# Kernel tuning notes

Hardware: AMD Instinct MI355X
Metric: run time of the kernel (lower is better)

## Reference

```python
import jax, jax.numpy as jnp
import numpy as np

N = 10000      # nodes
E = 160000     # edges (before self loops)
F_IN = 512     # in_features
F_OUT = 256    # out_features
SLOPE = 0.2    # LeakyReLU negative slope (PyG GATConv default)
EPS = 1e-12    # F.normalize eps


def setup_inputs() -> dict:
    key = jax.random.key(0)
    ks = jax.random.split(key, 14)
    feat = jax.random.normal(ks[0], (N, F_IN), jnp.float32)
    feat_a = jax.random.normal(ks[1], (N, F_IN), jnp.float32)
    edge_index = jax.random.randint(ks[2], (2, E), 0, N, dtype=jnp.int32)
    # binary neighborhood mask; diagonal set so every row has >=1 entry
    gn = (jax.random.uniform(ks[3], (N, N)) < 0.0016).astype(jnp.float32)
    graph_neigh = gn.at[jnp.arange(N), jnp.arange(N)].set(1.0)
    s1 = 1.0 / np.sqrt(F_IN)
    s2 = 1.0 / np.sqrt(F_OUT)
    return {
        "feat": feat,
        "feat_a": feat_a,
        "edge_index": edge_index,
        "graph_neigh": graph_neigh,
        # conv1: GATConv(F_IN -> F_OUT, heads=1)
        "W1": jax.random.normal(ks[4], (F_OUT, F_IN), jnp.float32) * s1,
        "att_src1": jax.random.normal(ks[5], (F_OUT,), jnp.float32) * s2,
        "att_dst1": jax.random.normal(ks[6], (F_OUT,), jnp.float32) * s2,
        "b1": jnp.zeros((F_OUT,), jnp.float32),
        # conv2: GATConv(F_OUT -> F_IN, heads=1)
        "W2": jax.random.normal(ks[7], (F_IN, F_OUT), jnp.float32) * s2,
        "att_src2": jax.random.normal(ks[8], (F_IN,), jnp.float32) * s1,
        "att_dst2": jax.random.normal(ks[9], (F_IN,), jnp.float32) * s1,
        "b2": jnp.zeros((F_IN,), jnp.float32),
        # discriminator bilinear
        "Wd": jax.random.normal(ks[10], (F_OUT, F_OUT), jnp.float32) * s2,
        "bd": jnp.zeros((), jnp.float32),
    }


def _gat_conv(x, src, dst, W, a_src, a_dst, b):
    # PyG GATConv, heads=1, concat=True, add_self_loops already applied.
    h = x @ W.T                       # [N, out]
    a_s = h @ a_src                   # [N]
    a_d = h @ a_dst                   # [N]
    e = a_s[src] + a_d[dst]           # [E+N]
    e = jnp.where(e > 0, e, SLOPE * e)  # leaky relu
    m = jax.ops.segment_max(e, dst, num_segments=N)
    p = jnp.exp(e - m[dst])
    s = jax.ops.segment_sum(p, dst, num_segments=N)
    coef = p / s[dst]                 # per-dst softmax over incoming edges
    out = jax.ops.segment_sum(coef[:, None] * h[src], dst, num_segments=N)
    return out + b


def reference(feat, feat_a, edge_index, graph_neigh, W1, att_src1, att_dst1, b1,
              W2, att_src2, att_dst2, b2, Wd, bd):
    loops = jnp.arange(N, dtype=edge_index.dtype)
    src = jnp.concatenate([edge_index[0], loops])
    dst = jnp.concatenate([edge_index[1], loops])

    z = _gat_conv(feat, src, dst, W1, att_src1, att_dst1, b1)      # [N, F_OUT]
    hiden_emb = z
    h = _gat_conv(z, src, dst, W2, att_src2, att_dst2, b2)         # [N, F_IN]
    emb = jax.nn.relu(z)
    z_a = _gat_conv(feat_a, src, dst, W1, att_src1, att_dst1, b1)
    emb_a = jax.nn.relu(z_a)

    def readout(e):
        vsum = graph_neigh @ e                                     # [N, F_OUT]
        row_sum = graph_neigh.sum(axis=1, keepdims=True)
        g = vsum / row_sum
        g = g / jnp.maximum(jnp.linalg.norm(g, axis=1, keepdims=True), EPS)
        return jax.nn.sigmoid(g)

    g = readout(emb)
    g_a = readout(emb_a)

    def bilin(x1, x2):
        return jnp.einsum('nd,de,ne->n', x1, Wd, x2)[:, None] + bd

    ret = jnp.concatenate([bilin(emb, g), bilin(emb_a, g)], axis=1)      # [N, 2]
    ret_a = jnp.concatenate([bilin(emb_a, g_a), bilin(emb, g_a)], axis=1)
    return (hiden_emb, h, ret, ret_a)
```

## Files before the change

kernel.cpp:

```cpp
#include <hip/hip_runtime.h>


#define N_NODES 10000
#define F_IN    512
#define F_OUT   256
#define SLOPE   0.2f

typedef unsigned short ushort_t;
typedef __attribute__((ext_vector_type(8))) short short8;
typedef __attribute__((ext_vector_type(4))) float f32x4;

__device__ __forceinline__ float bf2f(ushort_t h) {
    union { unsigned u; float f; } v;
    v.u = ((unsigned)h) << 16;
    return v.f;
}
__device__ __forceinline__ ushort_t f2bf(float f) {
    union { float f; unsigned u; } v; v.f = f;
    unsigned r = v.u + 0x7FFFu + ((v.u >> 16) & 1u);
    return (ushort_t)(r >> 16);
}
__device__ __forceinline__ float ldin(const void* p, size_t i, int isf32) {
    return isf32 ? ((const float*)p)[i] : bf2f(((const ushort_t*)p)[i]);
}

__global__ void detect_zero_kernel(int* counter) { counter[0] = 0; }

__global__ __launch_bounds__(256) void detect_count_kernel(const unsigned* __restrict__ p,
                                                           int* counter) {
    __shared__ int cnt;
    if (threadIdx.x == 0) cnt = 0;
    __syncthreads();
    int stride = gridDim.x * 256;
    int c = 0;
    for (int i = blockIdx.x * 256 + threadIdx.x; i < 1000000; i += stride) {
        unsigned u = p[i];
        unsigned h[2] = { u & 0xFFFFu, u >> 16 };
#pragma unroll
        for (int q = 0; q < 2; q++) {
            unsigned e = (h[q] >> 7) & 0xFFu;
            if ((h[q] & 0x7FFFu) != 0 && (e == 0xFFu || e < 0x60u)) c++;
        }
    }
    atomicAdd(&cnt, c);
    __syncthreads();
    if (threadIdx.x == 0) atomicAdd(counter, cnt);
}

__global__ void detect_final_kernel(const int* counter, int* flag) {
    flag[0] = (counter[0] > 10000) ? 1 : 0;
}

__global__ void zero2_kernel(int* p1, int n1, int* p2, int n2) {
    int i = blockIdx.x * 256 + threadIdx.x;
    if (i < n1) p1[i] = 0;
    if (i < n2) p2[i] = 0;
}

__global__ void hist_kernel(const int* __restrict__ dst, int E, int n, int* deg) {
    int i = blockIdx.x * 256 + threadIdx.x;
    if (i < E) {
        int d = dst[i];
        d = d < 0 ? 0 : (d >= n ? n - 1 : d);
        atomicAdd(&deg[d], 1);
    }
}

__global__ __launch_bounds__(1024) void scan_kernel(const int* __restrict__ deg,
                                                    int* row_ptr, int* cursor, int n) {
    __shared__ int wsum[16];
    __shared__ int carry_s;
    int tid = threadIdx.x;
    int lane = tid & 63, wid = tid >> 6;
    if (tid == 0) carry_s = 0;
    __syncthreads();
    for (int base = 0; base < n; base += 1024) {
        int i = base + tid;
        int x = (i < n) ? (deg[i] + 1) : 0;
        int incl = x;
#pragma unroll
        for (int off = 1; off < 64; off <<= 1) {
            int v = __shfl_up(incl, off);
            if (lane >= off) incl += v;
        }
        int carry = carry_s;
        if (lane == 63) wsum[wid] = incl;
        __syncthreads();
        if (wid == 0 && lane < 16) {
            int w = wsum[lane];
            int winc = w;
#pragma unroll
            for (int off = 1; off < 16; off <<= 1) {
                int v = __shfl_up(winc, off);
                if (lane >= off) winc += v;
            }
            wsum[lane] = winc - w;
            if (lane == 15) carry_s = carry + winc;
        }
        __syncthreads();
        int excl = carry + wsum[wid] + (incl - x);
        if (i < n) { row_ptr[i] = excl; cursor[i] = excl; }
        __syncthreads();
    }
    if (tid == 0) row_ptr[n] = carry_s;
}

__global__ void fill_kernel(const int* __restrict__ src, const int* __restrict__ dst,
                            int E, int n, int* cursor, int* col, int cap) {
    int i = blockIdx.x * 256 + threadIdx.x;
    if (i < E) {
        int d = dst[i];
        d = d < 0 ? 0 : (d >= n ? n - 1 : d);
        int s = src[i];
        s = s < 0 ? 0 : (s >= n ? n - 1 : s);
        int p = atomicAdd(&cursor[d], 1);
        if (p >= 0 && p < cap) col[p] = s;
    } else if (i < E + n) {
        int v = i - E;
        int p = atomicAdd(&cursor[v], 1);
        if (p >= 0 && p < cap) col[p] = v;
    }
}

#define BM 64
#define BN 64
#define BK 32

__device__ __forceinline__ uint4 pack8(const float* p) {
    float4 x = ((const float4*)p)[0];
    float4 y = ((const float4*)p)[1];
    uint4 r;
    r.x = (unsigned)f2bf(x.x) | ((unsigned)f2bf(x.y) << 16);
    r.y = (unsigned)f2bf(x.z) | ((unsigned)f2bf(x.w) << 16);
    r.z = (unsigned)f2bf(y.x) | ((unsigned)f2bf(y.y) << 16);
    r.w = (unsigned)f2bf(y.z) | ((unsigned)f2bf(y.w) << 16);
    return r;
}

__global__ __launch_bounds__(256) void gemm_bt(const void* __restrict__ Av,
                                               const void* __restrict__ Bv,
                                               ushort_t* __restrict__ C,
                                               int M, int N, int K,
                                               const int* __restrict__ flagp,
                                               int amode, int bmode) {
    __shared__ __align__(16) ushort_t As[BM * BK];
    __shared__ __align__(16) ushort_t Bs[BN * BK];
    int isf = flagp[0];
    int fA = (amode == 2) ? 1 : (amode ? isf : 0);
    int fB = (bmode == 2) ? 1 : (bmode ? isf : 0);
    int m0 = blockIdx.x * BM;
    int n0 = blockIdx.y * BN;
    int tid = threadIdx.x;
    int wave = tid >> 6, lane = tid & 63;
    int quad = lane >> 4, r16 = lane & 15;

    f32x4 acc[4] = {};

    int srow = tid >> 2;
    int schunk = tid & 3;
    int a_row = m0 + srow; if (a_row >= M) a_row = M - 1;
    int b_row = n0 + srow;
    const ushort_t* Ah = (const ushort_t*)Av + (size_t)a_row * K;
    const float*    Af = (const float*)Av    + (size_t)a_row * K;
    const ushort_t* Bh = (const ushort_t*)Bv + (size_t)b_row * K;
    const float*    Bf = (const float*)Bv    + (size_t)b_row * K;
    int s_sw = srow * BK + ((schunk ^ (srow & 3)) * 8);

    for (int k0 = 0; k0 < K; k0 += BK) {
        int eoff = k0 + schunk * 8;
        uint4 av = fA ? pack8(Af + eoff) : ((const uint4*)Ah)[eoff >> 3];
        uint4 bv = fB ? pack8(Bf + eoff) : ((const uint4*)Bh)[eoff >> 3];
        __syncthreads();
        *(uint4*)&As[s_sw] = av;
        *(uint4*)&Bs[s_sw] = bv;
        __syncthreads();
        int am = wave * 16 + r16;
        short8 a = *(const short8*)&As[am * BK + ((quad ^ (am & 3)) * 8)];
#pragma unroll
        for (int i = 0; i < 4; i++) {
            int bn = i * 16 + r16;
            short8 b = *(const short8*)&Bs[bn * BK + ((quad ^ (bn & 3)) * 8)];
            acc[i] = __builtin_amdgcn_mfma_f32_16x16x32_bf16(a, b, acc[i], 0, 0, 0);
        }
    }
    int m_base = m0 + wave * 16 + quad * 4;
#pragma unroll
    for (int i = 0; i < 4; i++) {
        int n = n0 + i * 16 + r16;
#pragma unroll
        for (int r = 0; r < 4; r++) {
            int m = m_base + r;
            if (m < M) C[(size_t)m * N + n] = f2bf(acc[i][r]);
        }
    }
}

__global__ __launch_bounds__(256) void attdot_kernel(const ushort_t* __restrict__ h,
                                                     const void* __restrict__ asrc,
                                                     const void* __restrict__ adst,
                                                     float* __restrict__ out_s,
                                                     float* __restrict__ out_d, int F,
                                                     int totR,
                                                     const int* __restrict__ flagp) {
    int isf = flagp[0];
    int row = blockIdx.x * 4 + (threadIdx.x >> 6);
    int lane = threadIdx.x & 63;
    if (row >= totR) return;
    const ushort_t* hr = h + (size_t)row * F;
    float ps = 0.f, pd = 0.f;
    for (int f = lane; f < F; f += 64) {
        float hv = bf2f(hr[f]);
        ps += hv * ldin(asrc, f, isf);
        pd += hv * ldin(adst, f, isf);
    }
    for (int off = 32; off; off >>= 1) {
        ps += __shfl_down(ps, off);
        pd += __shfl_down(pd, off);
    }
    if (lane == 0) { out_s[row] = ps; out_d[row] = pd; }
}

__global__ __launch_bounds__(256) void row_conv2(const int* __restrict__ row_ptr,
                                                 const int* __restrict__ col,
                                                 const float* __restrict__ a_s,
                                                 const float* __restrict__ a_d,
                                                 const ushort_t* __restrict__ h,
                                                 const void* __restrict__ bias,
                                                 int F, int nfirst,
                                                 float* out0, ushort_t* out1,
                                                 const int* __restrict__ flagp) {
    int isf = flagp[0];
    int b = blockIdx.x;
    int sel = (b >= nfirst) ? 1 : 0;
    int n = b - sel * nfirst;
    size_t roff = (size_t)sel * nfirst;
    int tid = threadIdx.x;
    int beg = row_ptr[n], end = row_ptr[n + 1];
    int deg = end - beg;
    float adn = a_d[roff + n];
    __shared__ float red[256];
    __shared__ float esh[2048];
    __shared__ int   csh[2048];

    float acc0 = 0.f, acc1 = 0.f;
    if (deg <= 2048) {
        float lm = -1e30f;
        for (int i = tid; i < deg; i += 256) {
            int c = col[beg + i];
            csh[i] = c;
            float e = a_s[roff + c] + adn;
            e = e > 0.f ? e : SLOPE * e;
            esh[i] = e;
            lm = fmaxf(lm, e);
        }
        red[tid] = lm; __syncthreads();
        for (int s = 128; s > 0; s >>= 1) { if (tid < s) red[tid] = fmaxf(red[tid], red[tid + s]); __syncthreads(); }
        float m = red[0]; __syncthreads();
        float lsum = 0.f;
        for (int i = tid; i < deg; i += 256) {
            float p = expf(esh[i] - m);
            esh[i] = p;
            lsum += p;
        }
        red[tid] = lsum; __syncthreads();
        for (int s = 128; s > 0; s >>= 1) { if (tid < s) red[tid] += red[tid + s]; __syncthreads(); }
        float denom = red[0];
        float inv_s = denom > 0.f ? 1.f / denom : 0.f;
        int j = 0;
        for (; j + 3 < deg; j += 4) {
            float w0 = esh[j], w1 = esh[j + 1], w2 = esh[j + 2], w3 = esh[j + 3];
            const ushort_t* p0 = h + (size_t)(roff + csh[j])     * F;
            const ushort_t* p1 = h + (size_t)(roff + csh[j + 1]) * F;
            const ushort_t* p2 = h + (size_t)(roff + csh[j + 2]) * F;
            const ushort_t* p3 = h + (size_t)(roff + csh[j + 3]) * F;
            acc0 += w0 * bf2f(p0[tid]) + w1 * bf2f(p1[tid])
                  + w2 * bf2f(p2[tid]) + w3 * bf2f(p3[tid]);
            if (F == 512)
                acc1 += w0 * bf2f(p0[tid + 256]) + w1 * bf2f(p1[tid + 256])
                      + w2 * bf2f(p2[tid + 256]) + w3 * bf2f(p3[tid + 256]);
        }
        for (; j < deg; j++) {
            float wj = esh[j];
            const ushort_t* p = h + (size_t)(roff + csh[j]) * F;
            acc0 += wj * bf2f(p[tid]);
            if (F == 512) acc1 += wj * bf2f(p[tid + 256]);
        }
        acc0 *= inv_s;
        acc1 *= inv_s;
    } else {
        float lm = -1e30f;
        for (int i = beg + tid; i < end; i += 256) {
            float e = a_s[roff + col[i]] + adn;
            e = e > 0.f ? e : SLOPE * e;
            lm = fmaxf(lm, e);
        }
        red[tid] = lm; __syncthreads();
        for (int s = 128; s > 0; s >>= 1) { if (tid < s) red[tid] = fmaxf(red[tid], red[tid + s]); __syncthreads(); }
        float m = red[0]; __syncthreads();
        float lsum = 0.f;
        for (int i = beg + tid; i < end; i += 256) {
            float e = a_s[roff + col[i]] + adn;
            e = e > 0.f ? e : SLOPE * e;
            lsum += expf(e - m);
        }
        red[tid] = lsum; __syncthreads();
        for (int s = 128; s > 0; s >>= 1) { if (tid < s) red[tid] += red[tid + s]; __syncthreads(); }
        float denom = red[0];
        float inv_s = denom > 0.f ? 1.f / denom : 0.f;
        __syncthreads();
        for (int c0 = beg; c0 < end; c0 += 256) {
            int i = c0 + tid;
            if (i < end) {
                float e = a_s[roff + col[i]] + adn;
                e = e > 0.f ? e : SLOPE * e;
                esh[tid] = expf(e - m) * inv_s;
                csh[tid] = col[i];
            }
            __syncthreads();
            int cnt = min(256, end - c0);
            for (int j = 0; j < cnt; j++) {
                float wj = esh[j];
                const ushort_t* hr = h + (size_t)(roff + csh[j]) * F;
                acc0 += wj * bf2f(hr[tid]);
                if (F == 512) acc1 += wj * bf2f(hr[tid + 256]);
            }
            __syncthreads();
        }
    }
    float z0 = acc0 + ldin(bias, tid, isf);
    if (sel == 0) { if (out0) out0[(size_t)n * F + tid] = z0; }
    else          { if (out1) out1[(size_t)n * F + tid] = f2bf(fmaxf(z0, 0.f)); }
    if (F == 512) {
        float z1 = acc1 + ldin(bias, tid + 256, isf);
        if (sel == 0) { if (out0) out0[(size_t)n * F + tid + 256] = z1; }
        else          { if (out1) out1[(size_t)n * F + tid + 256] = f2bf(fmaxf(z1, 0.f)); }
    }
}

__global__ __launch_bounds__(256) void readout_kernel(const void* __restrict__ gn,
                                                      const float* __restrict__ z,
                                                      const ushort_t* __restrict__ embA,
                                                      ushort_t* __restrict__ g,
                                                      ushort_t* __restrict__ ga,
                                                      const int* __restrict__ flagp) {
    int isf = flagp[0];
    int n = blockIdx.x, tid = threadIdx.x;
    __shared__ int list[2048];
    __shared__ int lcnt, tot;
    __shared__ float red[256];
    if (tid == 0) { lcnt = 0; tot = 0; }
    __syncthreads();
    const uint4* rowp = isf
        ? (const uint4*)((const float*)gn + (size_t)n * N_NODES)
        : (const uint4*)((const ushort_t*)gn + (size_t)n * N_NODES);
    const int NU4 = isf ? (N_NODES / 4) : (N_NODES / 8);
    float acc0 = 0.f, acc1 = 0.f;
    for (int base = 0; base < NU4; base += 256) {
        int idx = base + tid;
        if (idx < NU4) {
            uint4 v = rowp[idx];
            unsigned a4[4] = { v.x, v.y, v.z, v.w };
            if (isf) {
#pragma unroll
                for (int q = 0; q < 4; q++)
                    if (a4[q] & 0x7FFFFFFFu) { int p = atomicAdd(&lcnt, 1); list[p] = idx * 4 + q; }
            } else {
#pragma unroll
                for (int q = 0; q < 4; q++) {
                    if (a4[q] & 0x7FFFu)         { int p = atomicAdd(&lcnt, 1); list[p] = idx * 8 + q * 2; }
                    if ((a4[q] >> 16) & 0x7FFFu) { int p = atomicAdd(&lcnt, 1); list[p] = idx * 8 + q * 2 + 1; }
                }
            }
        }
        __syncthreads();
        int c = lcnt;
        int j = 0;
        for (; j + 3 < c; j += 4) {
            int i0 = list[j], i1 = list[j + 1], i2 = list[j + 2], i3 = list[j + 3];
            acc0 += fmaxf(z[(size_t)i0 * 256 + tid], 0.f) + fmaxf(z[(size_t)i1 * 256 + tid], 0.f)
                  + fmaxf(z[(size_t)i2 * 256 + tid], 0.f) + fmaxf(z[(size_t)i3 * 256 + tid], 0.f);
            acc1 += bf2f(embA[(size_t)i0 * 256 + tid]) + bf2f(embA[(size_t)i1 * 256 + tid])
                  + bf2f(embA[(size_t)i2 * 256 + tid]) + bf2f(embA[(size_t)i3 * 256 + tid]);
        }
        for (; j < c; j++) {
            int node = list[j];
            acc0 += fmaxf(z[(size_t)node * 256 + tid], 0.f);
            acc1 += bf2f(embA[(size_t)node * 256 + tid]);
        }
        __syncthreads();
        if (tid == 0) { tot += lcnt; lcnt = 0; }
        __syncthreads();
    }
    float cnt = (float)(tot > 0 ? tot : 1);
    float u0 = acc0 / cnt, u1 = acc1 / cnt;
    red[tid] = u0 * u0; __syncthreads();
    for (int s = 128; s > 0; s >>= 1) { if (tid < s) red[tid] += red[tid + s]; __syncthreads(); }
    float n0 = red[0]; __syncthreads();
    red[tid] = u1 * u1; __syncthreads();
    for (int s = 128; s > 0; s >>= 1) { if (tid < s) red[tid] += red[tid + s]; __syncthreads(); }
    float n1 = red[0];
    float g0 = u0 / fmaxf(sqrtf(n0), 1e-12f);
    float g1 = u1 / fmaxf(sqrtf(n1), 1e-12f);
    g0 = 1.f / (1.f + expf(-g0));
    g1 = 1.f / (1.f + expf(-g1));
    g[(size_t)n * 256 + tid]  = f2bf(g0);
    ga[(size_t)n * 256 + tid] = f2bf(g1);
}

__global__ __launch_bounds__(256) void bilin_kernel(const float* __restrict__ z,
                                                    const ushort_t* __restrict__ embA,
                                                    const ushort_t* __restrict__ Q,
                                                    const ushort_t* __restrict__ Qa,
                                                    const void* __restrict__ bdp,
                                                    float* __restrict__ ret,
                                                    float* __restrict__ ret_a,
                                                    const int* __restrict__ flagp) {
    int isf = flagp[0];
    int row = blockIdx.x * 4 + (threadIdx.x >> 6);
    int lane = threadIdx.x & 63;
    if (row >= N_NODES) return;
    const float*    zr = z    + (size_t)row * 256;
    const ushort_t* er = embA + (size_t)row * 256;
    const ushort_t* q  = Q    + (size_t)row * 256;
    const ushort_t* qa = Qa   + (size_t)row * 256;
    float d00 = 0, d01 = 0, d10 = 0, d11 = 0;
    for (int d = lane; d < 256; d += 64) {
        float em = fmaxf(zr[d], 0.f);
        float ea = bf2f(er[d]);
        float qv = bf2f(q[d]), qav = bf2f(qa[d]);
        d00 += em * qv;
        d01 += ea * qv;
        d10 += ea * qav;
        d11 += em * qav;
    }
    for (int off = 32; off; off >>= 1) {
        d00 += __shfl_down(d00, off);
        d01 += __shfl_down(d01, off);
        d10 += __shfl_down(d10, off);
        d11 += __shfl_down(d11, off);
    }
    if (lane == 0) {
        float bd = ldin(bdp, 0, isf);
        ret[row * 2]       = d00 + bd;
        ret[row * 2 + 1]   = d01 + bd;
        ret_a[row * 2]     = d10 + bd;
        ret_a[row * 2 + 1] = d11 + bd;
    }
}

extern "C" void kernel_launch(void* const* d_in, const int* in_sizes, int n_in,
                              void* d_out, int out_size, void* d_ws, size_t ws_size,
                              hipStream_t stream) {
    const void* feat    = d_in[0];
    const void* feat_a  = d_in[1];
    const int*  eidx    = (const int*)d_in[2];
    const void* gn      = d_in[3];
    const void* W1      = d_in[4];
    const void* asrc1   = d_in[5];
    const void* adst1   = d_in[6];
    const void* b1      = d_in[7];
    const void* W2      = d_in[8];
    const void* asrc2   = d_in[9];
    const void* adst2   = d_in[10];
    const void* b2      = d_in[11];
    const void* Wd      = d_in[12];
    const void* bd      = d_in[13];

    const int N = N_NODES;
    const int E = in_sizes[2] / 2;
    const int* src = eidx;
    const int* dst = eidx + E;

    float* out_z    = (float*)d_out;
    float* out_h    = out_z + (size_t)N * F_OUT;
    float* out_ret  = out_h + (size_t)N * F_IN;
    float* out_reta = out_ret + (size_t)N * 2;

    size_t off = 0;
    char* wsb = (char*)d_ws;
    auto carve = [&](size_t bytes) -> void* {
        void* p = wsb + off;
        off = (off + bytes + 255) & ~(size_t)255;
        return p;
    };
    ushort_t* R1   = (ushort_t*)carve((size_t)2 * N * 256 * 2);
    ushort_t* R2   = (ushort_t*)carve((size_t)2 * N * 256 * 2);
    ushort_t* embA = (ushort_t*)carve((size_t)N * 256 * 2);
    float* as1cat = (float*)carve((size_t)2 * N * 4);
    float* ad1cat = (float*)carve((size_t)2 * N * 4);
    float* as2    = (float*)carve((size_t)N * 4);
    float* ad2    = (float*)carve((size_t)N * 4);
    int* deg     = (int*)carve((size_t)N * 4);
    int* cursor  = (int*)carve((size_t)N * 4);
    int* row_ptr = (int*)carve((size_t)(N + 1) * 4);
    int* colb    = (int*)carve((size_t)(E + N) * 4);
    int* counter = (int*)carve(2 * sizeof(int));
    int* flag    = counter + 1;

    ushort_t* h1cat = R1;
    ushort_t* h2    = R1;
    ushort_t* gbuf  = R1;
    ushort_t* gabuf = R1 + (size_t)N * 256;
    ushort_t* Qb    = R2;
    ushort_t* Qab   = R2 + (size_t)N * 256;

    detect_zero_kernel<<<1, 1, 0, stream>>>(counter);
    detect_count_kernel<<<256, 256, 0, stream>>>((const unsigned*)feat, counter);
    detect_final_kernel<<<1, 1, 0, stream>>>(counter, flag);

    zero2_kernel<<<(E + N + 255) / 256, 256, 0, stream>>>(deg, N, colb, E + N);
    hist_kernel<<<(E + 255) / 256, 256, 0, stream>>>(dst, E, N, deg);
    scan_kernel<<<1, 1024, 0, stream>>>(deg, row_ptr, cursor, N);
    fill_kernel<<<(E + N + 255) / 256, 256, 0, stream>>>(src, dst, E, N, cursor, colb, E + N);

    const int MT  = (N + BM - 1) / BM;
    const int MT2 = (2 * N + BM - 1) / BM;

    gemm_bt<<<dim3(MT, F_OUT / BN), 256, 0, stream>>>(feat,   W1, h1cat,                  N, F_OUT, F_IN, flag, 1, 1);
    gemm_bt<<<dim3(MT, F_OUT / BN), 256, 0, stream>>>(feat_a, W1, h1cat + (size_t)N * 256, N, F_OUT, F_IN, flag, 1, 1);
    attdot_kernel<<<(2 * N + 3) / 4, 256, 0, stream>>>(h1cat, asrc1, adst1, as1cat, ad1cat, F_OUT, 2 * N, flag);
    row_conv2<<<2 * N, 256, 0, stream>>>(row_ptr, colb, as1cat, ad1cat, h1cat, b1, F_OUT, N, out_z, embA, flag);

    gemm_bt<<<dim3(MT, F_IN / BN), 256, 0, stream>>>(out_z, W2, h2, N, F_IN, F_OUT, flag, 2, 1);
    attdot_kernel<<<(N + 3) / 4, 256, 0, stream>>>(h2, asrc2, adst2, as2, ad2, F_IN, N, flag);
    row_conv2<<<N, 256, 0, stream>>>(row_ptr, colb, as2, ad2, h2, b2, F_IN, N, out_h, nullptr, flag);

    readout_kernel<<<N, 256, 0, stream>>>(gn, out_z, embA, gbuf, gabuf, flag);

    gemm_bt<<<dim3(MT2, 256 / BN), 256, 0, stream>>>(R1, Wd, R2, 2 * N, 256, 256, flag, 0, 1);
    bilin_kernel<<<(N + 3) / 4, 256, 0, stream>>>(out_z, embA, Qb, Qab, bd, out_ret, out_reta, flag);
}
```

Measured before the change: 827.0 us.

## Drop dtype detection, merge first-layer GEMMs, use wave-shuffle reductions

```diff
diff --git a/kernel.cpp b/kernel.cpp
--- a/kernel.cpp
+++ b/kernel.cpp
@@ -19,36 +19,6 @@
     union { float f; unsigned u; } v; v.f = f;
     unsigned r = v.u + 0x7FFFu + ((v.u >> 16) & 1u);
     return (ushort_t)(r >> 16);
-}
-__device__ __forceinline__ float ldin(const void* p, size_t i, int isf32) {
-    return isf32 ? ((const float*)p)[i] : bf2f(((const ushort_t*)p)[i]);
-}
-
-__global__ void detect_zero_kernel(int* counter) { counter[0] = 0; }
-
-__global__ __launch_bounds__(256) void detect_count_kernel(const unsigned* __restrict__ p,
-                                                           int* counter) {
-    __shared__ int cnt;
-    if (threadIdx.x == 0) cnt = 0;
-    __syncthreads();
-    int stride = gridDim.x * 256;
-    int c = 0;
-    for (int i = blockIdx.x * 256 + threadIdx.x; i < 1000000; i += stride) {
-        unsigned u = p[i];
-        unsigned h[2] = { u & 0xFFFFu, u >> 16 };
-#pragma unroll
-        for (int q = 0; q < 2; q++) {
-            unsigned e = (h[q] >> 7) & 0xFFu;
-            if ((h[q] & 0x7FFFu) != 0 && (e == 0xFFu || e < 0x60u)) c++;
-        }
-    }
-    atomicAdd(&cnt, c);
-    __syncthreads();
-    if (threadIdx.x == 0) atomicAdd(counter, cnt);
-}
-
-__global__ void detect_final_kernel(const int* counter, int* flag) {
-    flag[0] = (counter[0] > 10000) ? 1 : 0;
 }
 
 __global__ void zero2_kernel(int* p1, int n1, int* p2, int n2) {
@@ -138,16 +108,16 @@
 }
 
 __global__ __launch_bounds__(256) void gemm_bt(const void* __restrict__ Av,
+                                               const void* __restrict__ Av2,
+                                               int msplit,
                                                const void* __restrict__ Bv,
                                                ushort_t* __restrict__ C,
                                                int M, int N, int K,
-                                               const int* __restrict__ flagp,
                                                int amode, int bmode) {
     __shared__ __align__(16) ushort_t As[BM * BK];
     __shared__ __align__(16) ushort_t Bs[BN * BK];
-    int isf = flagp[0];
-    int fA = (amode == 2) ? 1 : (amode ? isf : 0);
-    int fB = (bmode == 2) ? 1 : (bmode ? isf : 0);
+    int fA = (amode == 2);
+    int fB = (bmode == 2);
     int m0 = blockIdx.x * BM;
     int n0 = blockIdx.y * BN;
     int tid = threadIdx.x;
@@ -159,9 +129,12 @@
     int srow = tid >> 2;
     int schunk = tid & 3;
     int a_row = m0 + srow; if (a_row >= M) a_row = M - 1;
+    int use2 = (a_row >= msplit);
+    const void* Abase = use2 ? Av2 : Av;
+    int arl = use2 ? (a_row - msplit) : a_row;
     int b_row = n0 + srow;
-    const ushort_t* Ah = (const ushort_t*)Av + (size_t)a_row * K;
-    const float*    Af = (const float*)Av    + (size_t)a_row * K;
+    const ushort_t* Ah = (const ushort_t*)Abase + (size_t)arl * K;
+    const float*    Af = (const float*)Abase    + (size_t)arl * K;
     const ushort_t* Bh = (const ushort_t*)Bv + (size_t)b_row * K;
     const float*    Bf = (const float*)Bv    + (size_t)b_row * K;
     int s_sw = srow * BK + ((schunk ^ (srow & 3)) * 8);
@@ -196,13 +169,11 @@
 }
 
 __global__ __launch_bounds__(256) void attdot_kernel(const ushort_t* __restrict__ h,
-                                                     const void* __restrict__ asrc,
-                                                     const void* __restrict__ adst,
+                                                     const float* __restrict__ asrc,
+                                                     const float* __restrict__ adst,
                                                      float* __restrict__ out_s,
                                                      float* __restrict__ out_d, int F,
-                                                     int totR,
-                                                     const int* __restrict__ flagp) {
-    int isf = flagp[0];
+                                                     int totR) {
     int row = blockIdx.x * 4 + (threadIdx.x >> 6);
     int lane = threadIdx.x & 63;
     if (row >= totR) return;
@@ -210,8 +181,8 @@
     float ps = 0.f, pd = 0.f;
     for (int f = lane; f < F; f += 64) {
         float hv = bf2f(hr[f]);
-        ps += hv * ldin(asrc, f, isf);
-        pd += hv * ldin(adst, f, isf);
+        ps += hv * asrc[f];
+        pd += hv * adst[f];
     }
     for (int off = 32; off; off >>= 1) {
         ps += __shfl_down(ps, off);
@@ -225,22 +196,23 @@
                                                  const float* __restrict__ a_s,
                                                  const float* __restrict__ a_d,
                                                  const ushort_t* __restrict__ h,
-                                                 const void* __restrict__ bias,
+                                                 const float* __restrict__ bias,
                                                  int F, int nfirst,
-                                                 float* out0, ushort_t* out1,
-                                                 const int* __restrict__ flagp) {
-    int isf = flagp[0];
+                                                 float* out0, ushort_t* outB,
+                                                 ushort_t* out1) {
     int b = blockIdx.x;
     int sel = (b >= nfirst) ? 1 : 0;
     int n = b - sel * nfirst;
     size_t roff = (size_t)sel * nfirst;
     int tid = threadIdx.x;
+    int lane = tid & 63, wid = tid >> 6;
     int beg = row_ptr[n], end = row_ptr[n + 1];
     int deg = end - beg;
     float adn = a_d[roff + n];
-    __shared__ float red[256];
     __shared__ float esh[2048];
     __shared__ int   csh[2048];
+    __shared__ float wred[8];
+    __shared__ float red[256];
 
     float acc0 = 0.f, acc1 = 0.f;
     if (deg <= 2048) {
@@ -253,18 +225,22 @@
             esh[i] = e;
             lm = fmaxf(lm, e);
         }
-        red[tid] = lm; __syncthreads();
-        for (int s = 128; s > 0; s >>= 1) { if (tid < s) red[tid] = fmaxf(red[tid], red[tid + s]); __syncthreads(); }
-        float m = red[0]; __syncthreads();
+#pragma unroll
+        for (int off = 32; off; off >>= 1) lm = fmaxf(lm, __shfl_down(lm, off));
+        if (lane == 0) wred[wid] = lm;
+        __syncthreads();
+        float m = fmaxf(fmaxf(wred[0], wred[1]), fmaxf(wred[2], wred[3]));
         float lsum = 0.f;
         for (int i = tid; i < deg; i += 256) {
             float p = expf(esh[i] - m);
             esh[i] = p;
             lsum += p;
         }
-        red[tid] = lsum; __syncthreads();
-        for (int s = 128; s > 0; s >>= 1) { if (tid < s) red[tid] += red[tid + s]; __syncthreads(); }
-        float denom = red[0];
+#pragma unroll
+        for (int off = 32; off; off >>= 1) lsum += __shfl_down(lsum, off);
+        if (lane == 0) wred[4 + wid] = lsum;
+        __syncthreads();
+        float denom = wred[4] + wred[5] + wred[6] + wred[7];
         float inv_s = denom > 0.f ? 1.f / denom : 0.f;
         int j = 0;
         for (; j + 3 < deg; j += 4) {
@@ -327,78 +303,75 @@
             __syncthreads();
         }
     }
-    float z0 = acc0 + ldin(bias, tid, isf);
-    if (sel == 0) { if (out0) out0[(size_t)n * F + tid] = z0; }
-    else          { if (out1) out1[(size_t)n * F + tid] = f2bf(fmaxf(z0, 0.f)); }
+    float z0 = acc0 + bias[tid];
+    if (sel == 0) {
+        if (out0) out0[(size_t)n * F + tid] = z0;
+        if (outB) outB[(size_t)n * F + tid] = f2bf(fmaxf(z0, 0.f));
+    } else {
+        if (out1) out1[(size_t)n * F + tid] = f2bf(fmaxf(z0, 0.f));
+    }
     if (F == 512) {
-        float z1 = acc1 + ldin(bias, tid + 256, isf);
-        if (sel == 0) { if (out0) out0[(size_t)n * F + tid + 256] = z1; }
-        else          { if (out1) out1[(size_t)n * F + tid + 256] = f2bf(fmaxf(z1, 0.f)); }
-    }
-}
-
-__global__ __launch_bounds__(256) void readout_kernel(const void* __restrict__ gn,
-                                                      const float* __restrict__ z,
+        float z1 = acc1 + bias[tid + 256];
+        if (sel == 0) {
+            if (out0) out0[(size_t)n * F + tid + 256] = z1;
+            if (outB) outB[(size_t)n * F + tid + 256] = f2bf(fmaxf(z1, 0.f));
+        } else {
+            if (out1) out1[(size_t)n * F + tid + 256] = f2bf(fmaxf(z1, 0.f));
+        }
+    }
+}
+
+#define RCAP 4096
+
+__global__ __launch_bounds__(256) void readout_kernel(const float* __restrict__ gn,
+                                                      const ushort_t* __restrict__ embB,
                                                       const ushort_t* __restrict__ embA,
                                                       ushort_t* __restrict__ g,
-                                                      ushort_t* __restrict__ ga,
-                                                      const int* __restrict__ flagp) {
-    int isf = flagp[0];
+                                                      ushort_t* __restrict__ ga) {
     int n = blockIdx.x, tid = threadIdx.x;
-    __shared__ int list[2048];
-    __shared__ int lcnt, tot;
-    __shared__ float red[256];
-    if (tid == 0) { lcnt = 0; tot = 0; }
+    int lane = tid & 63, wid = tid >> 6;
+    __shared__ int list[RCAP];
+    __shared__ int lcnt;
+    __shared__ float wred[8];
+    if (tid == 0) lcnt = 0;
     __syncthreads();
-    const uint4* rowp = isf
-        ? (const uint4*)((const float*)gn + (size_t)n * N_NODES)
-        : (const uint4*)((const ushort_t*)gn + (size_t)n * N_NODES);
-    const int NU4 = isf ? (N_NODES / 4) : (N_NODES / 8);
+    const uint4* rowp = (const uint4*)(gn + (size_t)n * N_NODES);
+    const int NU4 = N_NODES / 4;
+    for (int idx = tid; idx < NU4; idx += 256) {
+        uint4 v = rowp[idx];
+        if (v.x & 0x7FFFFFFFu) { int p = atomicAdd(&lcnt, 1); if (p < RCAP) list[p] = idx * 4; }
+        if (v.y & 0x7FFFFFFFu) { int p = atomicAdd(&lcnt, 1); if (p < RCAP) list[p] = idx * 4 + 1; }
+        if (v.z & 0x7FFFFFFFu) { int p = atomicAdd(&lcnt, 1); if (p < RCAP) list[p] = idx * 4 + 2; }
+        if (v.w & 0x7FFFFFFFu) { int p = atomicAdd(&lcnt, 1); if (p < RCAP) list[p] = idx * 4 + 3; }
+    }
+    __syncthreads();
+    int c = min(lcnt, RCAP);
     float acc0 = 0.f, acc1 = 0.f;
-    for (int base = 0; base < NU4; base += 256) {
-        int idx = base + tid;
-        if (idx < NU4) {
-            uint4 v = rowp[idx];
-            unsigned a4[4] = { v.x, v.y, v.z, v.w };
-            if (isf) {
-#pragma unroll
-                for (int q = 0; q < 4; q++)
-                    if (a4[q] & 0x7FFFFFFFu) { int p = atomicAdd(&lcnt, 1); list[p] = idx * 4 + q; }
-            } else {
-#pragma unroll
-                for (int q = 0; q < 4; q++) {
-                    if (a4[q] & 0x7FFFu)         { int p = atomicAdd(&lcnt, 1); list[p] = idx * 8 + q * 2; }
-                    if ((a4[q] >> 16) & 0x7FFFu) { int p = atomicAdd(&lcnt, 1); list[p] = idx * 8 + q * 2 + 1; }
-                }
-            }
-        }
-        __syncthreads();
-        int c = lcnt;
-        int j = 0;
-        for (; j + 3 < c; j += 4) {
-            int i0 = list[j], i1 = list[j + 1], i2 = list[j + 2], i3 = list[j + 3];
-            acc0 += fmaxf(z[(size_t)i0 * 256 + tid], 0.f) + fmaxf(z[(size_t)i1 * 256 + tid], 0.f)
-                  + fmaxf(z[(size_t)i2 * 256 + tid], 0.f) + fmaxf(z[(size_t)i3 * 256 + tid], 0.f);
-            acc1 += bf2f(embA[(size_t)i0 * 256 + tid]) + bf2f(embA[(size_t)i1 * 256 + tid])
-                  + bf2f(embA[(size_t)i2 * 256 + tid]) + bf2f(embA[(size_t)i3 * 256 + tid]);
-        }
-        for (; j < c; j++) {
-            int node = list[j];
-            acc0 += fmaxf(z[(size_t)node * 256 + tid], 0.f);
-            acc1 += bf2f(embA[(size_t)node * 256 + tid]);
-        }
-        __syncthreads();
-        if (tid == 0) { tot += lcnt; lcnt = 0; }
-        __syncthreads();
-    }
-    float cnt = (float)(tot > 0 ? tot : 1);
+    int j = 0;
+    for (; j + 3 < c; j += 4) {
+        int i0 = list[j], i1 = list[j + 1], i2 = list[j + 2], i3 = list[j + 3];
+        acc0 += bf2f(embB[(size_t)i0 * 256 + tid]) + bf2f(embB[(size_t)i1 * 256 + tid])
+              + bf2f(embB[(size_t)i2 * 256 + tid]) + bf2f(embB[(size_t)i3 * 256 + tid]);
+        acc1 += bf2f(embA[(size_t)i0 * 256 + tid]) + bf2f(embA[(size_t)i1 * 256 + tid])
+              + bf2f(embA[(size_t)i2 * 256 + tid]) + bf2f(embA[(size_t)i3 * 256 + tid]);
+    }
+    for (; j < c; j++) {
+        int node = list[j];
+        acc0 += bf2f(embB[(size_t)node * 256 + tid]);
+        acc1 += bf2f(embA[(size_t)node * 256 + tid]);
+    }
+    float cnt = (float)(c > 0 ? c : 1);
     float u0 = acc0 / cnt, u1 = acc1 / cnt;
-    red[tid] = u0 * u0; __syncthreads();
-    for (int s = 128; s > 0; s >>= 1) { if (tid < s) red[tid] += red[tid + s]; __syncthreads(); }
-    float n0 = red[0]; __syncthreads();
-    red[tid] = u1 * u1; __syncthreads();
-    for (int s = 128; s > 0; s >>= 1) { if (tid < s) red[tid] += red[tid + s]; __syncthreads(); }
-    float n1 = red[0];
+    float s0 = u0 * u0, s1 = u1 * u1;
+#pragma unroll
+    for (int off = 32; off; off >>= 1) {
+        s0 += __shfl_down(s0, off);
+        s1 += __shfl_down(s1, off);
+    }
+    if (lane == 0) { wred[wid] = s0; wred[4 + wid] = s1; }
+    __syncthreads();
+    float n0 = wred[0] + wred[1] + wred[2] + wred[3];
+    float n1 = wred[4] + wred[5] + wred[6] + wred[7];
     float g0 = u0 / fmaxf(sqrtf(n0), 1e-12f);
     float g1 = u1 / fmaxf(sqrtf(n1), 1e-12f);
     g0 = 1.f / (1.f + expf(-g0));
@@ -411,11 +384,9 @@
                                                     const ushort_t* __restrict__ embA,
                                                     const ushort_t* __restrict__ Q,
                                                     const ushort_t* __restrict__ Qa,
-                                                    const void* __restrict__ bdp,
+                                                    const float* __restrict__ bdp,
                                                     float* __restrict__ ret,
-                                                    float* __restrict__ ret_a,
-                                                    const int* __restrict__ flagp) {
-    int isf = flagp[0];
+                                                    float* __restrict__ ret_a) {
     int row = blockIdx.x * 4 + (threadIdx.x >> 6);
     int lane = threadIdx.x & 63;
     if (row >= N_NODES) return;
@@ -440,7 +411,7 @@
         d11 += __shfl_down(d11, off);
     }
     if (lane == 0) {
-        float bd = ldin(bdp, 0, isf);
+        float bd = bdp[0];
         ret[row * 2]       = d00 + bd;
         ret[row * 2 + 1]   = d01 + bd;
         ret_a[row * 2]     = d10 + bd;
@@ -451,20 +422,20 @@
 extern "C" void kernel_launch(void* const* d_in, const int* in_sizes, int n_in,
                               void* d_out, int out_size, void* d_ws, size_t ws_size,
                               hipStream_t stream) {
-    const void* feat    = d_in[0];
-    const void* feat_a  = d_in[1];
-    const int*  eidx    = (const int*)d_in[2];
-    const void* gn      = d_in[3];
-    const void* W1      = d_in[4];
-    const void* asrc1   = d_in[5];
-    const void* adst1   = d_in[6];
-    const void* b1      = d_in[7];
-    const void* W2      = d_in[8];
-    const void* asrc2   = d_in[9];
-    const void* adst2   = d_in[10];
-    const void* b2      = d_in[11];
-    const void* Wd      = d_in[12];
-    const void* bd      = d_in[13];
+    const void*  feat    = d_in[0];
+    const void*  feat_a  = d_in[1];
+    const int*   eidx    = (const int*)d_in[2];
+    const float* gn      = (const float*)d_in[3];
+    const void*  W1      = d_in[4];
+    const float* asrc1   = (const float*)d_in[5];
+    const float* adst1   = (const float*)d_in[6];
+    const float* b1      = (const float*)d_in[7];
+    const void*  W2      = d_in[8];
+    const float* asrc2   = (const float*)d_in[9];
+    const float* adst2   = (const float*)d_in[10];
+    const float* b2      = (const float*)d_in[11];
+    const void*  Wd      = d_in[12];
+    const float* bd      = (const float*)d_in[13];
 
     const int N = N_NODES;
     const int E = in_sizes[2] / 2;
@@ -486,6 +457,7 @@
     ushort_t* R1   = (ushort_t*)carve((size_t)2 * N * 256 * 2);
     ushort_t* R2   = (ushort_t*)carve((size_t)2 * N * 256 * 2);
     ushort_t* embA = (ushort_t*)carve((size_t)N * 256 * 2);
+    ushort_t* embB = (ushort_t*)carve((size_t)N * 256 * 2);
     float* as1cat = (float*)carve((size_t)2 * N * 4);
     float* ad1cat = (float*)carve((size_t)2 * N * 4);
     float* as2    = (float*)carve((size_t)N * 4);
@@ -494,8 +466,6 @@
     int* cursor  = (int*)carve((size_t)N * 4);
     int* row_ptr = (int*)carve((size_t)(N + 1) * 4);
     int* colb    = (int*)carve((size_t)(E + N) * 4);
-    int* counter = (int*)carve(2 * sizeof(int));
-    int* flag    = counter + 1;
 
     ushort_t* h1cat = R1;
     ushort_t* h2    = R1;
@@ -504,10 +474,6 @@
     ushort_t* Qb    = R2;
     ushort_t* Qab   = R2 + (size_t)N * 256;
 
-    detect_zero_kernel<<<1, 1, 0, stream>>>(counter);
-    detect_count_kernel<<<256, 256, 0, stream>>>((const unsigned*)feat, counter);
-    detect_final_kernel<<<1, 1, 0, stream>>>(counter, flag);
-
     zero2_kernel<<<(E + N + 255) / 256, 256, 0, stream>>>(deg, N, colb, E + N);
     hist_kernel<<<(E + 255) / 256, 256, 0, stream>>>(dst, E, N, deg);
     scan_kernel<<<1, 1024, 0, stream>>>(deg, row_ptr, cursor, N);
@@ -516,17 +482,21 @@
     const int MT  = (N + BM - 1) / BM;
     const int MT2 = (2 * N + BM - 1) / BM;
 
-    gemm_bt<<<dim3(MT, F_OUT / BN), 256, 0, stream>>>(feat,   W1, h1cat,                  N, F_OUT, F_IN, flag, 1, 1);
-    gemm_bt<<<dim3(MT, F_OUT / BN), 256, 0, stream>>>(feat_a, W1, h1cat + (size_t)N * 256, N, F_OUT, F_IN, flag, 1, 1);
-    attdot_kernel<<<(2 * N + 3) / 4, 256, 0, stream>>>(h1cat, asrc1, adst1, as1cat, ad1cat, F_OUT, 2 * N, flag);
-    row_conv2<<<2 * N, 256, 0, stream>>>(row_ptr, colb, as1cat, ad1cat, h1cat, b1, F_OUT, N, out_z, embA, flag);
-
-    gemm_bt<<<dim3(MT, F_IN / BN), 256, 0, stream>>>(out_z, W2, h2, N, F_IN, F_OUT, flag, 2, 1);
-    attdot_kernel<<<(N + 3) / 4, 256, 0, stream>>>(h2, asrc2, adst2, as2, ad2, F_IN, N, flag);
-    row_conv2<<<N, 256, 0, stream>>>(row_ptr, colb, as2, ad2, h2, b2, F_IN, N, out_h, nullptr, flag);
-
-    readout_kernel<<<N, 256, 0, stream>>>(gn, out_z, embA, gbuf, gabuf, flag);
-
-    gemm_bt<<<dim3(MT2, 256 / BN), 256, 0, stream>>>(R1, Wd, R2, 2 * N, 256, 256, flag, 0, 1);
-    bilin_kernel<<<(N + 3) / 4, 256, 0, stream>>>(out_z, embA, Qb, Qab, bd, out_ret, out_reta, flag);
-}
+    gemm_bt<<<dim3(MT2, F_OUT / BN), 256, 0, stream>>>(feat, feat_a, N, W1, h1cat,
+                                                       2 * N, F_OUT, F_IN, 2, 2);
+    attdot_kernel<<<(2 * N + 3) / 4, 256, 0, stream>>>(h1cat, asrc1, adst1, as1cat, ad1cat, F_OUT, 2 * N);
+    row_conv2<<<2 * N, 256, 0, stream>>>(row_ptr, colb, as1cat, ad1cat, h1cat, b1,
+                                         F_OUT, N, out_z, embB, embA);
+
+    gemm_bt<<<dim3(MT, F_IN / BN), 256, 0, stream>>>(out_z, out_z, N, W2, h2,
+                                                     N, F_IN, F_OUT, 2, 2);
+    attdot_kernel<<<(N + 3) / 4, 256, 0, stream>>>(h2, asrc2, adst2, as2, ad2, F_IN, N);
+    row_conv2<<<N, 256, 0, stream>>>(row_ptr, colb, as2, ad2, h2, b2,
+                                     F_IN, N, out_h, nullptr, nullptr);
+
+    readout_kernel<<<N, 256, 0, stream>>>(gn, embB, embA, gbuf, gabuf);
+
+    gemm_bt<<<dim3(MT2, 256 / BN), 256, 0, stream>>>(R1, R1, 2 * N, Wd, R2,
+                                                     2 * N, 256, 256, 0, 2);
+    bilin_kernel<<<(N + 3) / 4, 256, 0, stream>>>(out_z, embA, Qb, Qab, bd, out_ret, out_reta);
+}
```

Result: faster. 777.3 us (-6.0%).
